# Performance work log

Hardware: AMD Instinct MI355X
Metric: run time of the kernel (lower is better)

Reference implementation:

```python
import jax, jax.numpy as jnp
import numpy as np

WIN = 7
SHIFT = 3
HEADS = 6
EPS = 1e-5


def _rel_pos_index(ws):
    coords = np.stack(np.meshgrid(np.arange(ws), np.arange(ws), indexing='ij')).reshape(2, -1)
    rel = (coords[:, :, None] - coords[:, None, :]).transpose(1, 2, 0)  # (N, N, 2)
    rel[..., 0] += ws - 1
    rel[..., 1] += ws - 1
    rel[..., 0] *= 2 * ws - 1
    return jnp.asarray(rel.sum(-1).reshape(-1))  # (N*N,)


def _attn_mask(H, W, ws, ss):
    img = np.zeros((H, W))
    sl = (slice(0, -ws), slice(-ws, -ss), slice(-ss, None))
    cnt = 0
    for hs in sl:
        for wss in sl:
            img[hs, wss] = cnt
            cnt += 1
    mw = img.reshape(H // ws, ws, W // ws, ws).transpose(0, 2, 1, 3).reshape(-1, ws * ws)
    am = mw[:, None, :] - mw[:, :, None]  # (nw, N, N): mw[j]-mw[i]
    return jnp.asarray(np.where(am != 0, -1e9, 0.0).astype(np.float32))


def _layernorm(x, g, b):
    mu = x.mean(-1, keepdims=True)
    var = ((x - mu) ** 2).mean(-1, keepdims=True)
    return (x - mu) * jax.lax.rsqrt(var + EPS) * g + b


def setup_inputs() -> dict:
    key = jax.random.key(0)
    ks = jax.random.split(key, 6)
    B, H, W, C = 4, 224, 224, 192
    return {
        'x': jax.random.normal(ks[0], (B, H * W, C), jnp.float32),
        'norm1_g': jnp.ones((C,), jnp.float32),
        'norm1_b': jnp.zeros((C,), jnp.float32),
        'qkv_w': jax.random.normal(ks[1], (C, 3 * C), jnp.float32) * 0.02,
        'qkv_b': jnp.zeros((3 * C,), jnp.float32),
        'rpb_table': jax.random.normal(ks[2], ((2 * WIN - 1) ** 2, HEADS), jnp.float32) * 0.02,
        'proj_w': jax.random.normal(ks[3], (C, C), jnp.float32) * 0.02,
        'proj_b': jnp.zeros((C,), jnp.float32),
        'norm2_g': jnp.ones((C,), jnp.float32),
        'norm2_b': jnp.zeros((C,), jnp.float32),
        'fc1_w': jax.random.normal(ks[4], (C, 4 * C), jnp.float32) * 0.02,
        'fc1_b': jnp.zeros((4 * C,), jnp.float32),
        'fc2_w': jax.random.normal(ks[5], (4 * C, C), jnp.float32) * 0.02,
        'fc2_b': jnp.zeros((C,), jnp.float32),
        'h': 224,
        'w': 224,
    }


def reference(x, norm1_g, norm1_b, qkv_w, qkv_b, rpb_table, proj_w, proj_b,
              norm2_g, norm2_b, fc1_w, fc1_b, fc2_w, fc2_b, h, w):
    B, L, C = x.shape
    ch = C // HEADS
    N = WIN * WIN
    nh, nw = h // WIN, w // WIN
    rel_idx = _rel_pos_index(WIN)
    mask = _attn_mask(h, w, WIN, SHIFT)  # (nh*nw, N, N)

    shortcut = x
    xn = _layernorm(x, norm1_g, norm1_b).reshape(B, h, w, C)
    xs = jnp.roll(xn, (-SHIFT, -SHIFT), axis=(1, 2))
    # window partition -> (B*nh*nw, N, C)
    xw = xs.reshape(B, nh, WIN, nw, WIN, C).transpose(0, 1, 3, 2, 4, 5).reshape(B * nh * nw, N, C)

    qkv = (xw @ qkv_w + qkv_b).reshape(-1, N, 3, HEADS, ch).transpose(2, 0, 3, 1, 4)
    q, k, v = qkv[0], qkv[1], qkv[2]  # (NW, HEADS, N, ch)
    scale = ch ** -0.5
    attn = jnp.einsum('whic,whjc->whij', q * scale, k)
    bias = rpb_table[rel_idx].reshape(N, N, HEADS).transpose(2, 0, 1)  # (HEADS, N, N)
    attn = attn + bias[None]
    attn = attn.reshape(B, nh * nw, HEADS, N, N) + mask[None, :, None]
    attn = jax.nn.softmax(attn, axis=-1).reshape(B * nh * nw, HEADS, N, N)

    out = jnp.einsum('whij,whjc->whic', attn, v).transpose(0, 2, 1, 3).reshape(-1, N, C)
    out = out @ proj_w + proj_b
    # window reverse + roll back
    out = out.reshape(B, nh, nw, WIN, WIN, C).transpose(0, 1, 3, 2, 4, 5).reshape(B, h, w, C)
    out = jnp.roll(out, (SHIFT, SHIFT), axis=(1, 2)).reshape(B, L, C)

    x = shortcut + out
    xn2 = _layernorm(x, norm2_g, norm2_b)
    hid = jax.nn.gelu(xn2 @ fc1_w + fc1_b, approximate=False)
    return x + (hid @ fc2_w + fc2_b)
```

## Files before the change

kernel.cpp:

```cpp
#include <hip/hip_runtime.h>
#include <stdint.h>

#define MB    50176
#define CDIM  192

typedef __attribute__((ext_vector_type(8))) short bf16x8;
typedef __attribute__((ext_vector_type(4))) float f32x4;

#define WFENCE do{ asm volatile("s_waitcnt lgkmcnt(0)" ::: "memory"); \
                   __builtin_amdgcn_sched_barrier(0); }while(0)

__device__ __forceinline__ float wsum(float v){
  #pragma unroll
  for (int m=32;m>=1;m>>=1) v += __shfl_xor(v,m,64);
  return v;
}
__device__ __forceinline__ float bfbits2f(uint32_t h){
  union{uint32_t u; float f;} x; x.u = h<<16; return x.f;
}
__device__ __forceinline__ uint16_t f2bfbits(float f){
  union{float ff; uint32_t u;} x; x.ff = f;
  return (uint16_t)((x.u + 0x7FFFu + ((x.u>>16)&1u)) >> 16);
}
__device__ __forceinline__ void gload16(const void* g, void* l){
  __builtin_amdgcn_global_load_lds(
      (const __attribute__((address_space(1))) uint32_t*)g,
      (__attribute__((address_space(3))) uint32_t*)l, 16, 0, 0);
}
__device__ __forceinline__ float fast_gelu(float v){
  float z = v*(1.5957691f + 0.07135481f*v*v);
  return v * __builtin_amdgcn_rcpf(1.f + __expf(-z));
}
__device__ __forceinline__ size_t row2tok(int r_g){
  int widx = r_g/49, tpos = r_g - widx*49;
  int b = widx>>10, rem = widx&1023;
  int h = (rem>>5)*7 + tpos/7 + 3; if (h>=224) h-=224;
  int w = (rem&31)*7 + (tpos - (tpos/7)*7) + 3; if (w>=224) w-=224;
  return (size_t)b*MB + (size_t)h*224 + w;
}

__global__ __launch_bounds__(256) void prep_kernel(
    const float* __restrict__ qkv_w, const float* __restrict__ proj_w,
    const float* __restrict__ fc1_w, const float* __restrict__ fc2_w,
    const float* __restrict__ rpb,
    uint16_t* __restrict__ qkvW, uint16_t* __restrict__ prjW,
    uint16_t* __restrict__ fc1W, uint16_t* __restrict__ fc2W,
    float* __restrict__ btbl){
  int idx = blockIdx.x*256 + threadIdx.x;
  if (idx < 110592){ int k=idx/576, n=idx-k*576; qkvW[n*192+k]=f2bfbits(qkv_w[idx]); return; }
  idx -= 110592;
  if (idx < 36864){ int k=idx/192, n=idx-k*192; prjW[n*192+k]=f2bfbits(proj_w[idx]); return; }
  idx -= 36864;
  if (idx < 147456){ int k=idx/768, n=idx-k*768; fc1W[n*192+k]=f2bfbits(fc1_w[idx]); return; }
  idx -= 147456;
  if (idx < 147456){ int k=idx/192, n=idx-k*192; fc2W[n*768+k]=f2bfbits(fc2_w[idx]); return; }
  idx -= 147456;
  if (idx >= 98304) return;
  int j = idx & 63, i = (idx>>6) & 63;
  int hd = (idx>>12) % 6, cls = (idx>>12)/6;
  float v = -1e9f;
  if (i < 49 && j < 49){
    int dh = i/7 - j/7, dw = i%7 - j%7;
    v = rpb[((dh+6)*13 + (dw+6))*6 + hd];
    int cH = cls>>1, cW = cls&1;
    int li = (cH ? (i/7 < 4 ? 1 : 2) : 0)*3 + (cW ? (i%7 < 4 ? 1 : 2) : 0);
    int lj = (cH ? (j/7 < 4 ? 1 : 2) : 0)*3 + (cW ? (j%7 < 4 ? 1 : 2) : 0);
    if (li != lj) v = -1e9f;
  }
  btbl[idx] = v;
}

__global__ __launch_bounds__(256) void ln1_kernel(
    const float* __restrict__ x, const float* __restrict__ g,
    const float* __restrict__ bt, uint16_t* __restrict__ dst, int row0){
  int wid_l = (int)((blockIdx.x*256u + threadIdx.x) >> 6);
  int lane  = threadIdx.x & 63;
  size_t sidx = row2tok(row0 + wid_l);
  const float* s = x + sidx*CDIM;
  float v0=s[lane], v1=s[lane+64], v2=s[lane+128];
  float mu  = wsum(v0+v1+v2) * (1.f/192.f);
  float var = wsum(v0*v0+v1*v1+v2*v2)*(1.f/192.f) - mu*mu;
  float rs  = rsqrtf(var + 1e-5f);
  uint16_t* d = dst + (size_t)wid_l*CDIM;
  d[lane]     = f2bfbits((v0-mu)*rs*g[lane]     + bt[lane]);
  d[lane+64]  = f2bfbits((v1-mu)*rs*g[lane+64]  + bt[lane+64]);
  d[lane+128] = f2bfbits((v2-mu)*rs*g[lane+128] + bt[lane+128]);
}

enum { EPI_QKV=0, EPI_FC1=2, EPI_FC2=3 };

template<int EPI, int K, int NN>
__global__ __launch_bounds__(256) void mgemm(
    const uint16_t* __restrict__ A, const uint16_t* __restrict__ WT,
    const float* __restrict__ bias, void* __restrict__ outp,
    const uint16_t* __restrict__ resid, int row0){
  __shared__ __attribute__((aligned(16))) char As[2][128*128];
  __shared__ __attribute__((aligned(16))) char Bs[2][64*128];
  __shared__ int tokt[128];
  const int tid  = threadIdx.x;
  const int lane = tid & 63;
  const int wid  = tid >> 6;
  const int brow = blockIdx.y * 128;
  const int bcol = blockIdx.x * 64;

  f32x4 acc[4][2];
  #pragma unroll
  for (int m=0;m<4;m++)
    #pragma unroll
    for (int n=0;n<2;n++) acc[m][n] = (f32x4){0.f,0.f,0.f,0.f};

  const int srow = lane >> 3;
  const int sg   = (lane & 7) ^ srow;
  const int wm = wid >> 1, wn = wid & 1;
  const int lrow16 = lane & 15, lkh = lane >> 4;

  if constexpr (EPI==EPI_FC2){
    if (tid < 128) tokt[tid] = (int)row2tok(row0 + brow + tid);
    asm volatile("s_waitcnt lgkmcnt(0)" ::: "memory");
  }

  #define STAGE(k0, Ad, Bd) do{ \
    _Pragma("unroll") \
    for (int c = 0; c < 4; c++){ \
      int ch = wid*4 + c; \
      gload16(A + (size_t)(brow + ch*8 + srow)*K + (k0) + sg*8, (Ad) + ch*1024); \
    } \
    _Pragma("unroll") \
    for (int c = 0; c < 2; c++){ \
      int ch = wid*2 + c; \
      gload16(WT + (size_t)(bcol + ch*8 + srow)*K + (k0) + sg*8, (Bd) + ch*1024); \
    } \
  }while(0)

  constexpr int NK = K/64;
  STAGE(0, As[0], Bs[0]);
  #pragma unroll
  for (int ki = 0; ki < NK; ki++){
    const int cur = ki & 1;
    if (ki+1 < NK){
      STAGE((ki+1)*64, As[cur^1], Bs[cur^1]);
      asm volatile("s_waitcnt vmcnt(6)" ::: "memory");
    } else {
      asm volatile("s_waitcnt vmcnt(0)" ::: "memory");
    }
    __builtin_amdgcn_s_barrier();
    __builtin_amdgcn_sched_barrier(0);

    bf16x8 af[4][2], bfr[2][2];
    #pragma unroll
    for (int m=0;m<4;m++)
      #pragma unroll
      for (int ks=0;ks<2;ks++){
        int arow = wm*64 + m*16 + lrow16;
        af[m][ks] = *(const bf16x8*)(As[cur] + arow*128 + (((ks*4+lkh) ^ (arow&7))<<4));
      }
    #pragma unroll
    for (int n=0;n<2;n++)
      #pragma unroll
      for (int ks=0;ks<2;ks++){
        int brn = wn*32 + n*16 + lrow16;
        bfr[n][ks] = *(const bf16x8*)(Bs[cur] + brn*128 + (((ks*4+lkh) ^ (brn&7))<<4));
      }
    #pragma unroll
    for (int m=0;m<4;m++)
      #pragma unroll
      for (int n=0;n<2;n++)
        #pragma unroll
        for (int ks=0;ks<2;ks++)
          acc[m][n] = __builtin_amdgcn_mfma_f32_16x16x32_bf16(
              af[m][ks], bfr[n][ks], acc[m][n], 0, 0, 0);
    if (ki+1 < NK) __builtin_amdgcn_s_barrier();
  }
  #undef STAGE

  float bi[2];
  #pragma unroll
  for (int n=0;n<2;n++) bi[n] = bias[bcol + wn*32 + n*16 + lrow16];
  #pragma unroll
  for (int m=0;m<4;m++){
    #pragma unroll
    for (int j=0;j<4;j++){
      int lr = wm*64 + m*16 + lkh*4 + j;
      int r  = brow + lr;
      if constexpr (EPI==EPI_QKV || EPI==EPI_FC1){
        #pragma unroll
        for (int n=0;n<2;n++){
          float v = acc[m][n][j] + bi[n];
          if constexpr (EPI==EPI_FC1)
            v = fast_gelu(v);
          ((uint16_t*)outp)[(size_t)r*NN + bcol + wn*32 + n*16 + lrow16] = f2bfbits(v);
        }
      } else {
        size_t pr = (size_t)tokt[lr]*CDIM;
        #pragma unroll
        for (int n=0;n<2;n++){
          size_t p = pr + bcol + wn*32 + n*16 + lrow16;
          ((float*)outp)[p] = acc[m][n][j] + bi[n] + bfbits2f(resid[p]);
        }
      }
    }
  }
}

__global__ __launch_bounds__(384) void proj_ln2(
    const uint16_t* __restrict__ A, const uint16_t* __restrict__ WT,
    const float* __restrict__ pbias, const float* __restrict__ x,
    const float* __restrict__ g2, const float* __restrict__ b2,
    uint16_t* __restrict__ x2out, uint16_t* __restrict__ ln2out, int row0){
  __shared__ __attribute__((aligned(16))) char As[64*128];
  __shared__ __attribute__((aligned(16))) char Bs[192*128];
  __shared__ float stats[3][64][2];
  __shared__ int tokt[64];
  const int tid  = threadIdx.x;
  const int lane = tid & 63;
  const int wid  = tid >> 6;
  const int pm = wid / 3, pn = wid - pm*3;
  const int brow = blockIdx.x * 64;
  const int srow = lane >> 3;
  const int sg   = (lane & 7) ^ srow;
  const int r16 = lane & 15, t4 = lane >> 4;

  if (tid < 64) tokt[tid] = (int)row2tok(row0 + brow + tid);
  __syncthreads();

  float xv[2][4][4];
  #pragma unroll
  for (int m=0;m<2;m++)
    #pragma unroll
    for (int j=0;j<4;j++){
      int lr = pm*32 + m*16 + t4*4 + j;
      const float* xp = x + (size_t)tokt[lr]*CDIM;
      #pragma unroll
      for (int n=0;n<4;n++) xv[m][j][n] = xp[pn*64 + n*16 + r16];
    }

  f32x4 acc[2][4];
  #pragma unroll
  for (int m=0;m<2;m++)
    #pragma unroll
    for (int n=0;n<4;n++) acc[m][n] = (f32x4){0.f,0.f,0.f,0.f};

  for (int k0 = 0; k0 < 192; k0 += 64){
    for (int ch = wid; ch < 8; ch += 6)
      gload16(A + (size_t)(brow + ch*8 + srow)*192 + k0 + sg*8, As + ch*1024);
    for (int ch = wid; ch < 24; ch += 6)
      gload16(WT + (size_t)(ch*8 + srow)*192 + k0 + sg*8, Bs + ch*1024);
    __syncthreads();

    bf16x8 af[2][2], bfr[4][2];
    #pragma unroll
    for (int m=0;m<2;m++)
      #pragma unroll
      for (int ks=0;ks<2;ks++){
        int arow = pm*32 + m*16 + r16;
        af[m][ks] = *(const bf16x8*)(As + arow*128 + (((ks*4+t4) ^ (arow&7))<<4));
      }
    #pragma unroll
    for (int n=0;n<4;n++)
      #pragma unroll
      for (int ks=0;ks<2;ks++){
        int brn = pn*64 + n*16 + r16;
        bfr[n][ks] = *(const bf16x8*)(Bs + brn*128 + (((ks*4+t4) ^ (brn&7))<<4));
      }
    #pragma unroll
    for (int m=0;m<2;m++)
      #pragma unroll
      for (int n=0;n<4;n++)
        #pragma unroll
        for (int ks=0;ks<2;ks++)
          acc[m][n] = __builtin_amdgcn_mfma_f32_16x16x32_bf16(
              af[m][ks], bfr[n][ks], acc[m][n], 0, 0, 0);
    __syncthreads();
  }

  float bi[4], g2v[4], b2v[4];
  #pragma unroll
  for (int n=0;n<4;n++){
    int c = pn*64 + n*16 + r16;
    bi[n] = pbias[c]; g2v[n] = g2[c]; b2v[n] = b2[c];
  }
  #pragma unroll
  for (int m=0;m<2;m++){
    #pragma unroll
    for (int j=0;j<4;j++){
      int lr = pm*32 + m*16 + t4*4 + j;
      size_t pr = (size_t)tokt[lr]*CDIM;
      float s1 = 0.f, s2 = 0.f;
      #pragma unroll
      for (int n=0;n<4;n++){
        int c = pn*64 + n*16 + r16;
        float y = acc[m][n][j] + bi[n] + xv[m][j][n];
        acc[m][n][j] = y;
        x2out[pr + c] = f2bfbits(y);
        s1 += y; s2 = fmaf(y, y, s2);
      }
      #pragma unroll
      for (int mk=1; mk<16; mk<<=1){
        s1 += __shfl_xor(s1, mk, 64);
        s2 += __shfl_xor(s2, mk, 64);
      }
      if (r16 == 0){ stats[pn][lr][0] = s1; stats[pn][lr][1] = s2; }
    }
  }
  __syncthreads();
  #pragma unroll
  for (int m=0;m<2;m++){
    #pragma unroll
    for (int j=0;j<4;j++){
      int lr = pm*32 + m*16 + t4*4 + j;
      float s1 = stats[0][lr][0] + stats[1][lr][0] + stats[2][lr][0];
      float s2 = stats[0][lr][1] + stats[1][lr][1] + stats[2][lr][1];
      float mu = s1*(1.f/192.f);
      float rs = rsqrtf(s2*(1.f/192.f) - mu*mu + 1e-5f);
      size_t wr = (size_t)(brow + lr)*CDIM;
      #pragma unroll
      for (int n=0;n<4;n++){
        int c = pn*64 + n*16 + r16;
        ln2out[wr + c] = f2bfbits((acc[m][n][j]-mu)*rs*g2v[n] + b2v[n]);
      }
    }
  }
}

__global__ __launch_bounds__(256) void attn_kernel(
    const uint16_t* __restrict__ qkv, const float* __restrict__ btbl,
    uint16_t* __restrict__ attnout, int win0){
  const int wv   = threadIdx.x >> 6;
  const int lane = threadIdx.x & 63;
  const int whd  = blockIdx.x*4 + wv;
  const int widx = whd/6, hd = whd - widx*6;
  const int r16 = lane & 15, t4 = lane >> 4;
  __shared__ uint16_t Vt[4][32][72];
  __shared__ uint16_t Pl[4][16][72];

  #pragma unroll
  for (int e=lane; e<32*16; e+=64){ Vt[wv][e>>4][48 + (e&15)] = 0; }
  for (int ch = lane; ch < 196; ch += 64){
    int j = ch >> 2, c0 = (ch&3)*8;
    const uint16_t* src = qkv + ((size_t)widx*49 + j)*576 + hd*32 + 384 + c0;
    uint4 v = *(const uint4*)src;
    uint32_t u[4] = {v.x, v.y, v.z, v.w};
    #pragma unroll
    for (int q=0;q<8;q++) Vt[wv][c0+q][j] = (uint16_t)(u[q>>1] >> ((q&1)*16));
  }

  bf16x8 kf[4];
  #pragma unroll
  for (int jt=0;jt<4;jt++)
    kf[jt] = *(const bf16x8*)(qkv + ((size_t)widx*49 + jt*16 + r16)*576 + hd*32 + 192 + t4*8);

  const int gw = win0 + widx;
  const int cls = ((((gw&1023)>>5)==31)<<1) | ((gw&31)==31);
  const float* tb = btbl + ((size_t)(cls*6 + hd) << 12);
  const float scale = 0.17677669529663689f;

  WFENCE;
  bf16x8 bv[2][2];
  #pragma unroll
  for (int ct=0;ct<2;ct++)
    #pragma unroll
    for (int ks=0;ks<2;ks++)
      bv[ct][ks] = *(const bf16x8*)&Vt[wv][ct*16 + r16][ks*32 + t4*8];

  #pragma unroll 2
  for (int it=0; it<4; it++){
    bf16x8 qf = *(const bf16x8*)(qkv + ((size_t)widx*49 + it*16 + r16)*576 + hd*32 + t4*8);
    f32x4 acc[4];
    #pragma unroll
    for (int jt=0;jt<4;jt++){
      acc[jt] = (f32x4){0.f,0.f,0.f,0.f};
      acc[jt] = __builtin_amdgcn_mfma_f32_16x16x32_bf16(kf[jt], qf, acc[jt], 0,0,0);
    }
    int i = it*16 + r16;
    float s[4][4];
    float m = -3.4e38f;
    #pragma unroll
    for (int jt=0;jt<4;jt++){
      float4 bvv = *(const float4*)(tb + i*64 + jt*16 + t4*4);
      float bb[4] = {bvv.x, bvv.y, bvv.z, bvv.w};
      #pragma unroll
      for (int r=0;r<4;r++){
        s[jt][r] = acc[jt][r]*scale + bb[r];
        m = fmaxf(m, s[jt][r]);
      }
    }
    m = fmaxf(m, __shfl_xor(m, 16, 64));
    m = fmaxf(m, __shfl_xor(m, 32, 64));
    float sum = 0.f;
    #pragma unroll
    for (int jt=0;jt<4;jt++)
      #pragma unroll
      for (int r=0;r<4;r++){
        s[jt][r] = __expf(s[jt][r] - m);
        sum += s[jt][r];
      }
    sum += __shfl_xor(sum, 16, 64);
    sum += __shfl_xor(sum, 32, 64);
    float inv = 1.f / sum;
    #pragma unroll
    for (int jt=0;jt<4;jt++){
      uint32_t lo = (uint32_t)f2bfbits(s[jt][0]*inv) | ((uint32_t)f2bfbits(s[jt][1]*inv) << 16);
      uint32_t hi = (uint32_t)f2bfbits(s[jt][2]*inv) | ((uint32_t)f2bfbits(s[jt][3]*inv) << 16);
      *(uint2*)&Pl[wv][r16][jt*16 + t4*4] = make_uint2(lo, hi);
    }
    asm volatile("s_waitcnt lgkmcnt(0)" ::: "memory");

    f32x4 o[2];
    o[0] = (f32x4){0.f,0.f,0.f,0.f};
    o[1] = (f32x4){0.f,0.f,0.f,0.f};
    #pragma unroll
    for (int ks=0;ks<2;ks++){
      bf16x8 pa = *(const bf16x8*)&Pl[wv][r16][ks*32 + t4*8];
      #pragma unroll
      for (int ct=0;ct<2;ct++)
        o[ct] = __builtin_amdgcn_mfma_f32_16x16x32_bf16(pa, bv[ct][ks], o[ct], 0,0,0);
    }
    #pragma unroll
    for (int r=0;r<4;r++){
      int i2 = it*16 + t4*4 + r;
      if (i2 < 49){
        size_t base = ((size_t)widx*49 + i2)*CDIM + hd*32;
        attnout[base + r16]      = f2bfbits(o[0][r]);
        attnout[base + 16 + r16] = f2bfbits(o[1][r]);
      }
    }
  }
}

extern "C" void kernel_launch(void* const* d_in, const int* in_sizes, int n_in,
                              void* d_out, int out_size, void* d_ws, size_t ws_size,
                              hipStream_t stream) {
  const float* x       = (const float*)d_in[0];
  const float* n1g     = (const float*)d_in[1];
  const float* n1b     = (const float*)d_in[2];
  const float* qkv_w   = (const float*)d_in[3];
  const float* qkv_b   = (const float*)d_in[4];
  const float* rpb     = (const float*)d_in[5];
  const float* proj_w  = (const float*)d_in[6];
  const float* proj_b  = (const float*)d_in[7];
  const float* n2g     = (const float*)d_in[8];
  const float* n2b     = (const float*)d_in[9];
  const float* fc1_w   = (const float*)d_in[10];
  const float* fc1_b   = (const float*)d_in[11];
  const float* fc2_w   = (const float*)d_in[12];
  const float* fc2_b   = (const float*)d_in[13];
  float* out = (float*)d_out;

  const int T = 200704;
  const size_t TBL = 221184 + 73728 + 294912 + 294912 + 393216;
  const size_t ABYTES  = (size_t)T*CDIM*2;
  size_t bq_bytes = (size_t)(T/2)*768*2;
  size_t need_full = ABYTES + bq_bytes + ABYTES + TBL;
  bool full = ws_size >= need_full;

  char* ws = (char*)d_ws;
  if (full){
    uint16_t* Abuf = (uint16_t*)ws;
    uint16_t* Bq   = (uint16_t*)(ws + ABYTES);
    uint16_t* X2   = (uint16_t*)(ws + ABYTES + bq_bytes);
    char* wbase    = ws + ABYTES + bq_bytes + ABYTES;
    uint16_t* qkvW = (uint16_t*)wbase;
    uint16_t* prjW = (uint16_t*)(wbase + 221184);
    uint16_t* fc1W = (uint16_t*)(wbase + 221184 + 73728);
    uint16_t* fc2W = (uint16_t*)(wbase + 221184 + 73728 + 294912);
    float*    btbl = (float*)(wbase + 221184 + 73728 + 294912 + 294912);

    prep_kernel<<<2112, 256, 0, stream>>>(qkv_w, proj_w, fc1_w, fc2_w, rpb,
                                          qkvW, prjW, fc1W, fc2W, btbl);
    const int H = T/2;
    ln1_kernel<<<T/4, 256, 0, stream>>>(x, n1g, n1b, Abuf, 0);
    for (int h=0; h<2; h++){
      uint16_t* Ah = Abuf + (size_t)h*H*CDIM;
      mgemm<EPI_QKV, 192, 576>
          <<<dim3(9, H/128), 256, 0, stream>>>(Ah, qkvW, qkv_b, (void*)Bq, nullptr, 0);
      attn_kernel<<<(H/49)*6/4, 256, 0, stream>>>(Bq, btbl, Ah, h*(H/49));
    }
    proj_ln2<<<T/64, 384, 0, stream>>>(Abuf, prjW, proj_b, x, n2g, n2b,
                                       X2, Abuf, 0);
    for (int h=0; h<2; h++){
      uint16_t* Ah = Abuf + (size_t)h*H*CDIM;
      mgemm<EPI_FC1, 192, 768>
          <<<dim3(12, H/128), 256, 0, stream>>>(Ah, fc1W, fc1_b, (void*)Bq, nullptr, 0);
      mgemm<EPI_FC2, 768, 192>
          <<<dim3(3, H/128), 256, 0, stream>>>(Bq, fc2W, fc2_b, (void*)out, X2, h*H);
    }
  } else {
    const int TC = MB, NW = TC/49;
    uint16_t* Abuf = (uint16_t*)ws;
    uint16_t* Bq   = (uint16_t*)(ws + (size_t)TC*CDIM*2);
    uint16_t* X2   = (uint16_t*)(ws + (size_t)TC*CDIM*2 + (size_t)TC*768*2);
    char* wbase    = ws + (size_t)TC*CDIM*2 + (size_t)TC*768*2 + ABYTES;
    uint16_t* qkvW = (uint16_t*)wbase;
    uint16_t* prjW = (uint16_t*)(wbase + 221184);
    uint16_t* fc1W = (uint16_t*)(wbase + 221184 + 73728);
    uint16_t* fc2W = (uint16_t*)(wbase + 221184 + 73728 + 294912);
    float*    btbl = (float*)(wbase + 221184 + 73728 + 294912 + 294912);

    prep_kernel<<<2112, 256, 0, stream>>>(qkv_w, proj_w, fc1_w, fc2_w, rpb,
                                          qkvW, prjW, fc1W, fc2W, btbl);
    for (int c = 0; c < 4; c++){
      int row0 = c*TC, win0 = row0/49;
      ln1_kernel<<<TC/4, 256, 0, stream>>>(x, n1g, n1b, Abuf, row0);
      mgemm<EPI_QKV, 192, 576>
          <<<dim3(9, TC/128), 256, 0, stream>>>(Abuf, qkvW, qkv_b, (void*)Bq, nullptr, 0);
      attn_kernel<<<NW*6/4, 256, 0, stream>>>(Bq, btbl, Abuf, win0);
      proj_ln2<<<TC/64, 384, 0, stream>>>(Abuf, prjW, proj_b, x, n2g, n2b,
                                          X2, Abuf, row0);
      mgemm<EPI_FC1, 192, 768>
          <<<dim3(12, TC/128), 256, 0, stream>>>(Abuf, fc1W, fc1_b, (void*)Bq, nullptr, 0);
      mgemm<EPI_FC2, 768, 192>
          <<<dim3(3, TC/128), 256, 0, stream>>>(Bq, fc2W, fc2_b, (void*)out, X2, row0);
    }
  }
}
```

Measured before the change: 739.5 us.

## Fuse FC1, GELU and FC2 into one MLP kernel keeping hidden chunks in LDS

Replaces the separate FC1 and FC2 GEMM launches with one mlp_kernel. Each 64-row block computes the hidden layer in chunks of 96, applies GELU, stores the chunk in shared memory and accumulates FC2 directly. This removes the global round trip of the 768-wide hidden tensor and shrinks the workspace. Weights are read straight from global memory rather than staged through LDS, and there are two barriers per chunk. proj_ln2 also drops its early prefetch of the residual x in favour of loading it in the epilogue.

```diff
diff --git a/kernel.cpp b/kernel.cpp
--- a/kernel.cpp
+++ b/kernel.cpp
@@ -87,16 +87,11 @@
   d[lane+128] = f2bfbits((v2-mu)*rs*g[lane+128] + bt[lane+128]);
 }
 
-enum { EPI_QKV=0, EPI_FC1=2, EPI_FC2=3 };
-
-template<int EPI, int K, int NN>
-__global__ __launch_bounds__(256) void mgemm(
+__global__ __launch_bounds__(256) void qkv_gemm(
     const uint16_t* __restrict__ A, const uint16_t* __restrict__ WT,
-    const float* __restrict__ bias, void* __restrict__ outp,
-    const uint16_t* __restrict__ resid, int row0){
+    const float* __restrict__ bias, uint16_t* __restrict__ outp){
   __shared__ __attribute__((aligned(16))) char As[2][128*128];
   __shared__ __attribute__((aligned(16))) char Bs[2][64*128];
-  __shared__ int tokt[128];
   const int tid  = threadIdx.x;
   const int lane = tid & 63;
   const int wid  = tid >> 6;
@@ -114,30 +109,24 @@
   const int wm = wid >> 1, wn = wid & 1;
   const int lrow16 = lane & 15, lkh = lane >> 4;
 
-  if constexpr (EPI==EPI_FC2){
-    if (tid < 128) tokt[tid] = (int)row2tok(row0 + brow + tid);
-    asm volatile("s_waitcnt lgkmcnt(0)" ::: "memory");
-  }
-
   #define STAGE(k0, Ad, Bd) do{ \
     _Pragma("unroll") \
     for (int c = 0; c < 4; c++){ \
       int ch = wid*4 + c; \
-      gload16(A + (size_t)(brow + ch*8 + srow)*K + (k0) + sg*8, (Ad) + ch*1024); \
+      gload16(A + (size_t)(brow + ch*8 + srow)*192 + (k0) + sg*8, (Ad) + ch*1024); \
     } \
     _Pragma("unroll") \
     for (int c = 0; c < 2; c++){ \
       int ch = wid*2 + c; \
-      gload16(WT + (size_t)(bcol + ch*8 + srow)*K + (k0) + sg*8, (Bd) + ch*1024); \
+      gload16(WT + (size_t)(bcol + ch*8 + srow)*192 + (k0) + sg*8, (Bd) + ch*1024); \
     } \
   }while(0)
 
-  constexpr int NK = K/64;
   STAGE(0, As[0], Bs[0]);
   #pragma unroll
-  for (int ki = 0; ki < NK; ki++){
+  for (int ki = 0; ki < 3; ki++){
     const int cur = ki & 1;
-    if (ki+1 < NK){
+    if (ki+1 < 3){
       STAGE((ki+1)*64, As[cur^1], Bs[cur^1]);
       asm volatile("s_waitcnt vmcnt(6)" ::: "memory");
     } else {
@@ -169,7 +158,7 @@
         for (int ks=0;ks<2;ks++)
           acc[m][n] = __builtin_amdgcn_mfma_f32_16x16x32_bf16(
               af[m][ks], bfr[n][ks], acc[m][n], 0, 0, 0);
-    if (ki+1 < NK) __builtin_amdgcn_s_barrier();
+    if (ki+1 < 3) __builtin_amdgcn_s_barrier();
   }
   #undef STAGE
 
@@ -180,24 +169,10 @@
   for (int m=0;m<4;m++){
     #pragma unroll
     for (int j=0;j<4;j++){
-      int lr = wm*64 + m*16 + lkh*4 + j;
-      int r  = brow + lr;
-      if constexpr (EPI==EPI_QKV || EPI==EPI_FC1){
-        #pragma unroll
-        for (int n=0;n<2;n++){
-          float v = acc[m][n][j] + bi[n];
-          if constexpr (EPI==EPI_FC1)
-            v = fast_gelu(v);
-          ((uint16_t*)outp)[(size_t)r*NN + bcol + wn*32 + n*16 + lrow16] = f2bfbits(v);
-        }
-      } else {
-        size_t pr = (size_t)tokt[lr]*CDIM;
-        #pragma unroll
-        for (int n=0;n<2;n++){
-          size_t p = pr + bcol + wn*32 + n*16 + lrow16;
-          ((float*)outp)[p] = acc[m][n][j] + bi[n] + bfbits2f(resid[p]);
-        }
-      }
+      int r = brow + wm*64 + m*16 + lkh*4 + j;
+      #pragma unroll
+      for (int n=0;n<2;n++)
+        outp[(size_t)r*576 + bcol + wn*32 + n*16 + lrow16] = f2bfbits(acc[m][n][j] + bi[n]);
     }
   }
 }
@@ -221,18 +196,6 @@
   const int r16 = lane & 15, t4 = lane >> 4;
 
   if (tid < 64) tokt[tid] = (int)row2tok(row0 + brow + tid);
-  __syncthreads();
-
-  float xv[2][4][4];
-  #pragma unroll
-  for (int m=0;m<2;m++)
-    #pragma unroll
-    for (int j=0;j<4;j++){
-      int lr = pm*32 + m*16 + t4*4 + j;
-      const float* xp = x + (size_t)tokt[lr]*CDIM;
-      #pragma unroll
-      for (int n=0;n<4;n++) xv[m][j][n] = xp[pn*64 + n*16 + r16];
-    }
 
   f32x4 acc[2][4];
   #pragma unroll
@@ -289,7 +252,7 @@
       #pragma unroll
       for (int n=0;n<4;n++){
         int c = pn*64 + n*16 + r16;
-        float y = acc[m][n][j] + bi[n] + xv[m][j][n];
+        float y = acc[m][n][j] + bi[n] + x[pr + c];
         acc[m][n][j] = y;
         x2out[pr + c] = f2bfbits(y);
         s1 += y; s2 = fmaf(y, y, s2);
@@ -317,6 +280,112 @@
       for (int n=0;n<4;n++){
         int c = pn*64 + n*16 + r16;
         ln2out[wr + c] = f2bfbits((acc[m][n][j]-mu)*rs*g2v[n] + b2v[n]);
+      }
+    }
+  }
+}
+
+__global__ __launch_bounds__(384) void mlp_kernel(
+    const uint16_t* __restrict__ A,
+    const uint16_t* __restrict__ W1T,
+    const uint16_t* __restrict__ W2T,
+    const float* __restrict__ b1, const float* __restrict__ b2,
+    const uint16_t* __restrict__ x2,
+    float* __restrict__ out, int row0){
+  __shared__ __attribute__((aligned(16))) char As[3*8192];
+  __shared__ uint16_t hid[64][104];
+  __shared__ int tokt[64];
+  const int tid  = threadIdx.x;
+  const int lane = tid & 63, wid = tid >> 6;
+  const int pm = wid / 3, pn = wid - pm*3;
+  const int r16 = lane & 15, t4 = lane >> 4;
+  const int brow = blockIdx.x * 64;
+  const int srow = lane >> 3;
+  const int sg   = (lane & 7) ^ srow;
+
+  if (tid < 64) tokt[tid] = (int)row2tok(row0 + brow + tid);
+
+  for (int idx = wid; idx < 24; idx += 6){
+    int kb = idx >> 3, ch = idx & 7;
+    gload16(A + (size_t)(brow + ch*8 + srow)*192 + kb*64 + sg*8,
+            As + kb*8192 + ch*1024);
+  }
+  __syncthreads();
+
+  f32x4 acc2[2][4];
+  #pragma unroll
+  for (int m=0;m<2;m++)
+    #pragma unroll
+    for (int n=0;n<4;n++) acc2[m][n] = (f32x4){0.f,0.f,0.f,0.f};
+
+  #pragma unroll 1
+  for (int hc = 0; hc < 8; hc++){
+    f32x4 acc1[2][2];
+    #pragma unroll
+    for (int m=0;m<2;m++)
+      #pragma unroll
+      for (int n=0;n<2;n++) acc1[m][n] = (f32x4){0.f,0.f,0.f,0.f};
+    #pragma unroll
+    for (int kk=0;kk<6;kk++){
+      bf16x8 bw[2];
+      #pragma unroll
+      for (int n=0;n<2;n++)
+        bw[n] = *(const bf16x8*)(W1T + (size_t)(hc*96 + pn*32 + n*16 + r16)*192 + kk*32 + t4*8);
+      bf16x8 af[2];
+      #pragma unroll
+      for (int m=0;m<2;m++){
+        int arow = pm*32 + m*16 + r16;
+        af[m] = *(const bf16x8*)(As + (kk>>1)*8192 + (arow>>3)*1024 + (arow&7)*128
+                                 + ((((kk&1)*4 + t4) ^ (arow&7))<<4));
+      }
+      #pragma unroll
+      for (int m=0;m<2;m++)
+        #pragma unroll
+        for (int n=0;n<2;n++)
+          acc1[m][n] = __builtin_amdgcn_mfma_f32_16x16x32_bf16(af[m], bw[n], acc1[m][n], 0,0,0);
+    }
+    #pragma unroll
+    for (int m=0;m<2;m++)
+      #pragma unroll
+      for (int n=0;n<2;n++){
+        float bb = b1[hc*96 + pn*32 + n*16 + r16];
+        #pragma unroll
+        for (int j=0;j<4;j++){
+          hid[pm*32 + m*16 + t4*4 + j][pn*32 + n*16 + r16] =
+              f2bfbits(fast_gelu(acc1[m][n][j] + bb));
+        }
+      }
+    __syncthreads();
+    #pragma unroll
+    for (int ks=0;ks<3;ks++){
+      bf16x8 pa[2];
+      #pragma unroll
+      for (int m=0;m<2;m++)
+        pa[m] = *(const bf16x8*)&hid[pm*32 + m*16 + r16][ks*32 + t4*8];
+      #pragma unroll
+      for (int n=0;n<4;n++){
+        bf16x8 bw2 = *(const bf16x8*)(W2T + (size_t)(pn*64 + n*16 + r16)*768 + hc*96 + ks*32 + t4*8);
+        #pragma unroll
+        for (int m=0;m<2;m++)
+          acc2[m][n] = __builtin_amdgcn_mfma_f32_16x16x32_bf16(pa[m], bw2, acc2[m][n], 0,0,0);
+      }
+    }
+    __syncthreads();
+  }
+
+  float b2v[4];
+  #pragma unroll
+  for (int n=0;n<4;n++) b2v[n] = b2[pn*64 + n*16 + r16];
+  #pragma unroll
+  for (int m=0;m<2;m++){
+    #pragma unroll
+    for (int j=0;j<4;j++){
+      int lr = pm*32 + m*16 + t4*4 + j;
+      size_t pr = (size_t)tokt[lr]*CDIM;
+      #pragma unroll
+      for (int n=0;n<4;n++){
+        size_t p = pr + pn*64 + n*16 + r16;
+        out[p] = acc2[m][n][j] + b2v[n] + bfbits2f(x2[p]);
       }
     }
   }
@@ -448,8 +517,8 @@
 
   const int T = 200704;
   const size_t TBL = 221184 + 73728 + 294912 + 294912 + 393216;
-  const size_t ABYTES  = (size_t)T*CDIM*2;
-  size_t bq_bytes = (size_t)(T/2)*768*2;
+  const size_t ABYTES = (size_t)T*CDIM*2;
+  size_t bq_bytes = (size_t)(T/2)*576*2;
   size_t need_full = ABYTES + bq_bytes + ABYTES + TBL;
   bool full = ws_size >= need_full;
 
@@ -471,25 +540,19 @@
     ln1_kernel<<<T/4, 256, 0, stream>>>(x, n1g, n1b, Abuf, 0);
     for (int h=0; h<2; h++){
       uint16_t* Ah = Abuf + (size_t)h*H*CDIM;
-      mgemm<EPI_QKV, 192, 576>
-          <<<dim3(9, H/128), 256, 0, stream>>>(Ah, qkvW, qkv_b, (void*)Bq, nullptr, 0);
+      qkv_gemm<<<dim3(9, H/128), 256, 0, stream>>>(Ah, qkvW, qkv_b, Bq);
       attn_kernel<<<(H/49)*6/4, 256, 0, stream>>>(Bq, btbl, Ah, h*(H/49));
     }
     proj_ln2<<<T/64, 384, 0, stream>>>(Abuf, prjW, proj_b, x, n2g, n2b,
                                        X2, Abuf, 0);
-    for (int h=0; h<2; h++){
-      uint16_t* Ah = Abuf + (size_t)h*H*CDIM;
-      mgemm<EPI_FC1, 192, 768>
-          <<<dim3(12, H/128), 256, 0, stream>>>(Ah, fc1W, fc1_b, (void*)Bq, nullptr, 0);
-      mgemm<EPI_FC2, 768, 192>
-          <<<dim3(3, H/128), 256, 0, stream>>>(Bq, fc2W, fc2_b, (void*)out, X2, h*H);
-    }
+    mlp_kernel<<<T/64, 384, 0, stream>>>(Abuf, fc1W, fc2W, fc1_b, fc2_b,
+                                         X2, out, 0);
   } else {
     const int TC = MB, NW = TC/49;
     uint16_t* Abuf = (uint16_t*)ws;
     uint16_t* Bq   = (uint16_t*)(ws + (size_t)TC*CDIM*2);
-    uint16_t* X2   = (uint16_t*)(ws + (size_t)TC*CDIM*2 + (size_t)TC*768*2);
-    char* wbase    = ws + (size_t)TC*CDIM*2 + (size_t)TC*768*2 + ABYTES;
+    uint16_t* X2   = (uint16_t*)(ws + (size_t)TC*CDIM*2 + (size_t)TC*576*2);
+    char* wbase    = ws + (size_t)TC*CDIM*2 + (size_t)TC*576*2 + ABYTES;
     uint16_t* qkvW = (uint16_t*)wbase;
     uint16_t* prjW = (uint16_t*)(wbase + 221184);
     uint16_t* fc1W = (uint16_t*)(wbase + 221184 + 73728);
@@ -501,15 +564,12 @@
     for (int c = 0; c < 4; c++){
       int row0 = c*TC, win0 = row0/49;
       ln1_kernel<<<TC/4, 256, 0, stream>>>(x, n1g, n1b, Abuf, row0);
-      mgemm<EPI_QKV, 192, 576>
-          <<<dim3(9, TC/128), 256, 0, stream>>>(Abuf, qkvW, qkv_b, (void*)Bq, nullptr, 0);
+      qkv_gemm<<<dim3(9, TC/128), 256, 0, stream>>>(Abuf, qkvW, qkv_b, Bq);
       attn_kernel<<<NW*6/4, 256, 0, stream>>>(Bq, btbl, Abuf, win0);
       proj_ln2<<<TC/64, 384, 0, stream>>>(Abuf, prjW, proj_b, x, n2g, n2b,
                                           X2, Abuf, row0);
-      mgemm<EPI_FC1, 192, 768>
-          <<<dim3(12, TC/128), 256, 0, stream>>>(Abuf, fc1W, fc1_b, (void*)Bq, nullptr, 0);
-      mgemm<EPI_FC2, 768, 192>
-          <<<dim3(3, TC/128), 256, 0, stream>>>(Bq, fc2W, fc2_b, (void*)out, X2, row0);
-    }
-  }
-}
+      mlp_kernel<<<TC/64, 384, 0, stream>>>(Abuf, fc1W, fc2W, fc1_b, fc2_b,
+                                            X2, out, row0);
+    }
+  }
+}
```

Result: slower. 856.5 us (+15.8%).
